# Kernel optimization log

Measured on AMD Instinct MI355X. Metric: run time of the kernel, lower is better.

The kernel has to match this reference:

```python
import jax, jax.numpy as jnp
import numpy as np

A = 14      # num abnormalities (hardcoded 14 W_Q Linears)
QD = 64     # query_dim
H = 12      # num_heads
CH = 768    # cls_hidden_dim == H * QD (required by residual add)
B = 4096    # batch


def _layernorm(x, g, b, eps=1e-5):
    m = jnp.mean(x, axis=-1, keepdims=True)
    v = jnp.mean((x - m) ** 2, axis=-1, keepdims=True)
    return (x - m) * jax.lax.rsqrt(v + eps) * g + b


def setup_inputs() -> dict:
    key = jax.random.key(0)
    ks = jax.random.split(key, 9)
    s = 0.02
    return dict(
        classification_queries=jax.random.normal(ks[0], (A, QD), dtype=jnp.float32),
        cls_token=jax.random.normal(ks[1], (B, A, CH), dtype=jnp.float32),
        WQ=jax.random.normal(ks[2], (A, QD, QD), dtype=jnp.float32) * s,  # 14 per-abnormality query projections
        bQ=jnp.zeros((A, QD), dtype=jnp.float32),
        WK=jax.random.normal(ks[3], (H, CH, QD), dtype=jnp.float32) * s,  # per-head K projections
        bK=jnp.zeros((H, QD), dtype=jnp.float32),
        WV=jax.random.normal(ks[4], (H, CH, QD), dtype=jnp.float32) * s,  # per-head V projections
        bV=jnp.zeros((H, QD), dtype=jnp.float32),
        W1=jax.random.normal(ks[5], (H * QD, CH), dtype=jnp.float32) * s,
        b1=jnp.zeros((CH,), dtype=jnp.float32),
        W2=jax.random.normal(ks[6], (CH, CH), dtype=jnp.float32) * s,
        b2=jnp.zeros((CH,), dtype=jnp.float32),
        g1=jnp.ones((CH,), dtype=jnp.float32),
        be1=jnp.zeros((CH,), dtype=jnp.float32),
        g2=jnp.ones((CH,), dtype=jnp.float32),
        be2=jnp.zeros((CH,), dtype=jnp.float32),
    )


def reference(classification_queries, cls_token, WQ, bQ, WK, bK, WV, bV,
              W1, b1, W2, b2, g1, be1, g2, be2):
    dt = cls_token.dtype
    scale = jnp.asarray(float(QD) ** 0.5, dt)
    # Per-abnormality query projection (batched over the 14 Linears): [A, QD]
    Q = jnp.einsum('ad,adq->aq', classification_queries, WQ) + bQ
    # Per-head K/V projections, batched over heads: [B, H, S, QD] with S == A == 14
    K = jnp.einsum('bsc,hcq->bhsq', cls_token, WK) + bK[None, :, None, :]
    V = jnp.einsum('bsc,hcq->bhsq', cls_token, WV) + bV[None, :, None, :]
    # Attention scores: [B, H, A, S]; Q is broadcast across batch (torch expand)
    scores = jnp.einsum('aq,bhsq->bhas', Q, K) / scale
    # NOTE: original applies softmax over dim=1 of [B, A, S] -> the query axis 'a'
    attn = jax.nn.softmax(scores, axis=2)
    # Weighted values, heads concatenated on last dim: [B, A, H*QD]
    out = jnp.einsum('bhas,bhsq->bahq', attn, V).reshape(cls_token.shape[0], A, H * QD)
    x = _layernorm(cls_token + out, g1, be1)
    ff = jnp.maximum(jnp.dot(x, W1) + b1, 0.0) @ W2 + b2
    return _layernorm(x + ff, g2, be2)
```

## Files before the change

### kernel.cpp

```cpp
#include <hip/hip_runtime.h>
#include <stdint.h>

#define B_  4096
#define A_  14
#define QD_ 64
#define H_  12
#define CH_ 768
#define M_  (B_*A_)
#define NS_ (H_*A_)
#define N1_ (CH_+NS_)

typedef float  f32x4  __attribute__((ext_vector_type(4)));
typedef short  bf16x8 __attribute__((ext_vector_type(8)));
typedef short  s16x4  __attribute__((ext_vector_type(4)));
typedef int    i32x4  __attribute__((ext_vector_type(4)));

#define GLOAD_LDS16(gp, lp) \
  __builtin_amdgcn_global_load_lds((const __attribute__((address_space(1))) void*)(gp), \
                                   (__attribute__((address_space(3))) void*)(lp), 16, 0, 0)

__device__ __forceinline__ float b2f(ushort u) {
  union { uint32_t u; float f; } c; c.u = ((uint32_t)u) << 16; return c.f;
}
__device__ __forceinline__ ushort f2b(float f) {
  union { float f; uint32_t u; } c; c.f = f;
  uint32_t u = c.u;
  return (ushort)((u + 0x7FFFu + ((u >> 16) & 1u)) >> 16);
}


__global__ void prep_q(const float* __restrict__ cq, const float* __restrict__ WQ,
                       const float* __restrict__ bQ, float* __restrict__ Qout) {
  for (int i = threadIdx.x; i < A_*QD_; i += 256) {
    int a = i >> 6, q = i & 63;
    float acc = bQ[i];
    for (int d = 0; d < 64; ++d) acc += cq[a*64 + d] * WQ[(a*64 + d)*64 + q];
    Qout[i] = acc;
  }
}

__global__ void prep_wcat(const float* __restrict__ WV, const float* __restrict__ bV,
                          const float* __restrict__ WK, const float* __restrict__ bK,
                          const float* __restrict__ Qb, ushort* __restrict__ Wcat,
                          float* __restrict__ biascat) {
  int n = blockIdx.x, t = threadIdx.x;
  if (n < CH_) {
    int h = n >> 6, q = n & 63;
    for (int c = t; c < CH_; c += 256)
      Wcat[(size_t)n*CH_ + c] = f2b(WV[((size_t)h*CH_ + c)*64 + q]);
    if (t == 0) biascat[n] = bV[n];
  } else if (n < N1_) {
    int j = n - CH_; int h = j / 14, a = j % 14;
    __shared__ float qrow[64];
    if (t < 64) qrow[t] = Qb[a*64 + t];
    __syncthreads();
    for (int c = t; c < CH_; c += 256) {
      const float* wk = WK + ((size_t)h*CH_ + c)*64;
      float acc = 0.f;
      #pragma unroll
      for (int q = 0; q < 64; ++q) acc += qrow[q] * wk[q];
      Wcat[(size_t)n*CH_ + c] = f2b(acc * 0.125f);
    }
    if (t == 0) {
      float acc = 0.f;
      for (int q = 0; q < 64; ++q) acc += qrow[q] * bK[h*64 + q];
      biascat[n] = acc * 0.125f;
    }
  } else {
    for (int c = t; c < CH_; c += 256) Wcat[(size_t)n*CH_ + c] = 0;
    if (t == 0) biascat[n] = 0.f;
  }
}

__global__ void prep_wt(const float* __restrict__ W1, const float* __restrict__ W2,
                        ushort* __restrict__ W1T, ushort* __restrict__ W2T) {
  int i = blockIdx.x;
  int n = (i < CH_) ? i : i - CH_;
  const float* W = (i < CH_) ? W1 : W2;
  ushort* O = (i < CH_) ? W1T : W2T;
  for (int k = threadIdx.x; k < CH_; k += 256)
    O[(size_t)n*CH_ + k] = f2b(W[(size_t)k*CH_ + n]);
}

__global__ void prep_cls(const float* __restrict__ cls, ushort* __restrict__ out) {
  const size_t n4 = (size_t)M_*CH_/4;
  for (size_t i = (size_t)blockIdx.x*256 + threadIdx.x; i < n4; i += (size_t)gridDim.x*256) {
    const float* p = cls + i*4;
    s16x4 o;
    o[0] = (short)f2b(p[0]); o[1] = (short)f2b(p[1]);
    o[2] = (short)f2b(p[2]); o[3] = (short)f2b(p[3]);
    *(s16x4*)(out + i*4) = o;
  }
}

template<int MODE>
__global__ __launch_bounds__(512, 2)
void gemm_k(const ushort* __restrict__ Ap, const ushort* __restrict__ Bp,
            const float* __restrict__ bias,
            ushort* __restrict__ Cb, float* __restrict__ Sout) {
  constexpr int GN  = (MODE == 0) ? 4 : 3;
  constexpr int NWG = 224 * GN;
  const int tid = threadIdx.x;
  const int wave = tid >> 6, lane = tid & 63;
  const int wm = wave >> 2, wn = wave & 3;

  const int bid = blockIdx.x;
  const int tl = (bid & 7) * (NWG >> 3) + (bid >> 3);
  const int m0 = (tl / GN) * 256, n0 = (tl % GN) * 256;

  __shared__ __align__(16) ushort Asm[2][256*64];
  __shared__ __align__(16) ushort Bsm[2][256*64];

  f32x4 acc[8][4] = {};

  const int tq = tid >> 3;
  const int gsc = (tid & 7) ^ (tq & 7);
  const ushort* Ab = Ap + (size_t)(m0 + tq)*CH_ + gsc*8;
  const ushort* Bb = Bp + (size_t)(n0 + tq)*CH_ + gsc*8;

  #define STAGE_TILE(slot, k0) do {                                         \
    _Pragma("unroll")                                                       \
    for (int q = 0; q < 4; ++q) {                                           \
      GLOAD_LDS16(Ab + (size_t)q*64*CH_ + (k0), &Asm[slot][q*4096 + wave*512]); \
      GLOAD_LDS16(Bb + (size_t)q*64*CH_ + (k0), &Bsm[slot][q*4096 + wave*512]); \
    }                                                                       \
  } while (0)

  STAGE_TILE(0, 0);

  for (int kt = 0; kt < 12; ++kt) {
    const int cur = kt & 1;
    if (kt < 11) {
      STAGE_TILE(cur ^ 1, (kt + 1) * 64);
      asm volatile("s_waitcnt vmcnt(8)" ::: "memory");
    } else {
      asm volatile("s_waitcnt vmcnt(0)" ::: "memory");
    }
    __builtin_amdgcn_sched_barrier(0);
    __builtin_amdgcn_s_barrier();
    __builtin_amdgcn_sched_barrier(0);

    const ushort* As = &Asm[cur][0];
    const ushort* Bs = &Bsm[cur][0];
    #pragma unroll
    for (int kk = 0; kk < 2; ++kk) {
      bf16x8 af[8], bfr[4];
      #pragma unroll
      for (int i = 0; i < 8; ++i) {
        int ar = wm*128 + i*16 + (lane & 15);
        int ab = (ar*128 + kk*64 + (lane >> 4)*16) ^ ((ar & 7) << 4);
        af[i] = *(const bf16x8*)((const char*)As + ab);
      }
      #pragma unroll
      for (int j = 0; j < 4; ++j) {
        int br = wn*64 + j*16 + (lane & 15);
        int bb = (br*128 + kk*64 + (lane >> 4)*16) ^ ((br & 7) << 4);
        bfr[j] = *(const bf16x8*)((const char*)Bs + bb);
      }
      __builtin_amdgcn_s_setprio(1);
      #pragma unroll
      for (int i = 0; i < 8; ++i)
        #pragma unroll
        for (int j = 0; j < 4; ++j)
          acc[i][j] = __builtin_amdgcn_mfma_f32_16x16x32_bf16(af[i], bfr[j], acc[i][j], 0, 0, 0);
      __builtin_amdgcn_s_setprio(0);
    }
    __builtin_amdgcn_sched_barrier(0);
    __builtin_amdgcn_s_barrier();
    __builtin_amdgcn_sched_barrier(0);
  }
  #undef STAGE_TILE

  #pragma unroll
  for (int j = 0; j < 4; ++j) {
    const int gc = n0 + wn*64 + j*16 + (lane & 15);
    const float bv = (MODE == 0 && gc >= N1_) ? 0.f : bias[gc];
    #pragma unroll
    for (int i = 0; i < 8; ++i) {
      const int gr0 = m0 + wm*128 + i*16 + ((lane >> 4) << 2);
      #pragma unroll
      for (int r = 0; r < 4; ++r) {
        const float v = acc[i][j][r] + bv;
        const int gr = gr0 + r;
        if (MODE == 0) {
          if (gc < CH_) {
            Cb[(size_t)gr*CH_ + gc] = f2b(v);
          } else if (gc < N1_) {
            const int j2 = gc - CH_;
            const int h = j2 / 14, a = j2 % 14;
            const int b = gr / 14, s = gr % 14;
            Sout[(((size_t)b*H_ + h)*A_ + a)*A_ + s] = v;
          }
        } else if (MODE == 1) {
          Cb[(size_t)gr*CH_ + gc] = f2b(fmaxf(v, 0.f));
        } else {
          Cb[(size_t)gr*CH_ + gc] = f2b(v);
        }
      }
    }
  }
}

__global__ __launch_bounds__(256)
void attn_ln1(const float* __restrict__ Sbuf, const ushort* __restrict__ Vbuf,
              const ushort* __restrict__ clsb, const float* __restrict__ g1,
              const float* __restrict__ be1, ushort* __restrict__ xout) {
  const int b = blockIdx.x, tid = threadIdx.x;
  const int wave = tid >> 6, lane = tid & 63;
  __shared__ __align__(16) float  s_sc[H_*A_*A_];
  __shared__ __align__(16) ushort s_v[A_*CH_];

  for (int i = tid; i < H_*A_*A_; i += 256) s_sc[i] = Sbuf[(size_t)b*H_*A_*A_ + i];
  for (int i = tid; i < A_*CH_/8; i += 256)
    *(i32x4*)((char*)s_v + i*16) = *(const i32x4*)((const char*)(Vbuf + (size_t)b*A_*CH_) + i*16);
  __syncthreads();

  if (tid < H_*A_) {
    int h = tid / 14, s = tid % 14;
    float vals[14], mx = -1e30f;
    #pragma unroll
    for (int a = 0; a < 14; ++a) { float v = s_sc[(h*14 + a)*14 + s]; vals[a] = v; mx = fmaxf(mx, v); }
    float sum = 0.f;
    #pragma unroll
    for (int a = 0; a < 14; ++a) { float e = __expf(vals[a] - mx); vals[a] = e; sum += e; }
    float inv = 1.f / sum;
    #pragma unroll
    for (int a = 0; a < 14; ++a) s_sc[(h*14 + a)*14 + s] = vals[a] * inv;
  }
  __syncthreads();

  for (int a = wave; a < A_; a += 4) {
    f32x4 vr[3]; float sum = 0.f, sq = 0.f;
    #pragma unroll
    for (int j = 0; j < 3; ++j) {
      const int c = (lane + j*64) * 4;
      const int h = c >> 6;
      const float* at = &s_sc[(h*14 + a)*14];
      f32x4 acc = {};
      #pragma unroll
      for (int s = 0; s < 14; ++s) {
        float w = at[s];
        s16x4 vv = *(const s16x4*)(&s_v[s*CH_ + c]);
        acc[0] += w * b2f((ushort)vv[0]); acc[1] += w * b2f((ushort)vv[1]);
        acc[2] += w * b2f((ushort)vv[2]); acc[3] += w * b2f((ushort)vv[3]);
      }
      s16x4 cv = *(const s16x4*)(clsb + ((size_t)b*A_ + a)*CH_ + c);
      f32x4 t;
      t[0] = b2f((ushort)cv[0]) + acc[0]; t[1] = b2f((ushort)cv[1]) + acc[1];
      t[2] = b2f((ushort)cv[2]) + acc[2]; t[3] = b2f((ushort)cv[3]) + acc[3];
      vr[j] = t;
      #pragma unroll
      for (int u = 0; u < 4; ++u) { sum += t[u]; sq += t[u]*t[u]; }
    }
    #pragma unroll
    for (int off = 32; off >= 1; off >>= 1) {
      sum += __shfl_xor(sum, off, 64);
      sq  += __shfl_xor(sq,  off, 64);
    }
    float mean = sum * (1.f/768.f);
    float var  = sq * (1.f/768.f) - mean*mean;
    float rstd = rsqrtf(var + 1e-5f);
    #pragma unroll
    for (int j = 0; j < 3; ++j) {
      int c = (lane + j*64)*4;
      f32x4 gv = *(const f32x4*)(g1 + c);
      f32x4 bv = *(const f32x4*)(be1 + c);
      s16x4 pk;
      #pragma unroll
      for (int u = 0; u < 4; ++u)
        pk[u] = (short)f2b((vr[j][u] - mean)*rstd*gv[u] + bv[u]);
      *(s16x4*)(&xout[((size_t)b*A_ + a)*CH_ + c]) = pk;
    }
  }
}

__global__ __launch_bounds__(256)
void ln2_k(const ushort* __restrict__ xb, const ushort* __restrict__ yb,
           const float* __restrict__ g2, const float* __restrict__ be2,
           float* __restrict__ out) {
  const int row = blockIdx.x*4 + (threadIdx.x >> 6);
  const int lane = threadIdx.x & 63;
  const ushort* xr = xb + (size_t)row*CH_;
  const ushort* yr = yb + (size_t)row*CH_;
  float v[12]; float sum = 0.f, sq = 0.f;
  #pragma unroll
  for (int j = 0; j < 3; ++j) {
    int c = (lane + j*64)*4;
    s16x4 xv = *(const s16x4*)(xr + c);
    s16x4 yv = *(const s16x4*)(yr + c);
    #pragma unroll
    for (int u = 0; u < 4; ++u) {
      float t = b2f((ushort)xv[u]) + b2f((ushort)yv[u]);
      v[j*4 + u] = t; sum += t; sq += t*t;
    }
  }
  #pragma unroll
  for (int off = 32; off >= 1; off >>= 1) {
    sum += __shfl_xor(sum, off, 64);
    sq  += __shfl_xor(sq,  off, 64);
  }
  float mean = sum * (1.f/768.f);
  float var  = sq * (1.f/768.f) - mean*mean;
  float rstd = rsqrtf(var + 1e-5f);
  float* orow = out + (size_t)row*CH_;
  #pragma unroll
  for (int j = 0; j < 3; ++j) {
    int c = (lane + j*64)*4;
    f32x4 gv = *(const f32x4*)(g2 + c);
    f32x4 bv = *(const f32x4*)(be2 + c);
    f32x4 o;
    #pragma unroll
    for (int u = 0; u < 4; ++u) o[u] = (v[j*4+u] - mean)*rstd*gv[u] + bv[u];
    *(f32x4*)(orow + c) = o;
  }
}

extern "C" void kernel_launch(void* const* d_in, const int* in_sizes, int n_in,
                              void* d_out, int out_size, void* d_ws, size_t ws_size,
                              hipStream_t stream) {
  const float* cq  = (const float*)d_in[0];
  const float* cls = (const float*)d_in[1];
  const float* WQ  = (const float*)d_in[2];
  const float* bQ  = (const float*)d_in[3];
  const float* WK  = (const float*)d_in[4];
  const float* bK  = (const float*)d_in[5];
  const float* WV  = (const float*)d_in[6];
  const float* bV  = (const float*)d_in[7];
  const float* W1  = (const float*)d_in[8];
  const float* b1  = (const float*)d_in[9];
  const float* W2  = (const float*)d_in[10];
  const float* b2  = (const float*)d_in[11];
  const float* g1  = (const float*)d_in[12];
  const float* be1 = (const float*)d_in[13];
  const float* g2  = (const float*)d_in[14];
  const float* be2 = (const float*)d_in[15];
  float* out = (float*)d_out;

  char* ws = (char*)d_ws;
  float*  qbuf    = (float*)(ws + 0);
  float*  biascat = (float*)(ws + 4096);
  ushort* wcat    = (ushort*)(ws + 8192);
  ushort* w1t     = (ushort*)(ws + 1581056);
  ushort* w2t     = (ushort*)(ws + 2760704);
  ushort* clsbf   = (ushort*)(ws + 4194304);
  ushort* vbuf    = (ushort*)(ws + 92274688);
  float*  sbuf    = (float*)(ws + 180355072);
  ushort* ybuf    = (ushort*)(ws + 218890240);
  ushort* xbuf  = clsbf;
  ushort* h1buf = vbuf;

  prep_q   <<<1,    256, 0, stream>>>(cq, WQ, bQ, qbuf);
  prep_wcat<<<1024, 256, 0, stream>>>(WV, bV, WK, bK, qbuf, wcat, biascat);
  prep_wt  <<<1536, 256, 0, stream>>>(W1, W2, w1t, w2t);
  prep_cls <<<2048, 256, 0, stream>>>(cls, clsbf);

  gemm_k<0><<<224*4, 512, 0, stream>>>(clsbf, wcat, biascat, vbuf, sbuf);
  attn_ln1 <<<B_, 256, 0, stream>>>(sbuf, vbuf, clsbf, g1, be1, xbuf);
  gemm_k<1><<<224*3, 512, 0, stream>>>(xbuf, w1t, b1, h1buf, nullptr);
  gemm_k<2><<<224*3, 512, 0, stream>>>(h1buf, w2t, b2, ybuf, nullptr);
  ln2_k    <<<M_/4, 256, 0, stream>>>(xbuf, ybuf, g2, be2, out);
}
```

Before: 740.4 us.

## Switch GEMM mainloop to triple-buffered K=32 tiles with interleaved prefetch

```diff
diff --git a/kernel.cpp b/kernel.cpp
--- a/kernel.cpp
+++ b/kernel.cpp
@@ -100,6 +100,7 @@
             ushort* __restrict__ Cb, float* __restrict__ Sout) {
   constexpr int GN  = (MODE == 0) ? 4 : 3;
   constexpr int NWG = 224 * GN;
+  constexpr int KT  = 24;
   const int tid = threadIdx.x;
   const int wave = tid >> 6, lane = tid & 63;
   const int wm = wave >> 2, wn = wave & 3;
@@ -108,68 +109,79 @@
   const int tl = (bid & 7) * (NWG >> 3) + (bid >> 3);
   const int m0 = (tl / GN) * 256, n0 = (tl % GN) * 256;
 
-  __shared__ __align__(16) ushort Asm[2][256*64];
-  __shared__ __align__(16) ushort Bsm[2][256*64];
+  __shared__ __align__(16) ushort Asm[3][256*32];
+  __shared__ __align__(16) ushort Bsm[3][256*32];
 
   f32x4 acc[8][4] = {};
 
-  const int tq = tid >> 3;
-  const int gsc = (tid & 7) ^ (tq & 7);
-  const ushort* Ab = Ap + (size_t)(m0 + tq)*CH_ + gsc*8;
-  const ushort* Bb = Bp + (size_t)(n0 + tq)*CH_ + gsc*8;
-
-  #define STAGE_TILE(slot, k0) do {                                         \
-    _Pragma("unroll")                                                       \
-    for (int q = 0; q < 4; ++q) {                                           \
-      GLOAD_LDS16(Ab + (size_t)q*64*CH_ + (k0), &Asm[slot][q*4096 + wave*512]); \
-      GLOAD_LDS16(Bb + (size_t)q*64*CH_ + (k0), &Bsm[slot][q*4096 + wave*512]); \
-    }                                                                       \
+  const int line0 = (wave*2 + 0)*8 + (lane >> 3);
+  const int line1 = (wave*2 + 1)*8 + (lane >> 3);
+  const int chS0 = (lane & 7) ^ (line0 & 7);
+  const int chS1 = (lane & 7) ^ (line1 & 7);
+  const int aoff0 = (2*line0 + (chS0 >> 2))*CH_ + (chS0 & 3)*8;
+  const int aoff1 = (2*line1 + (chS1 >> 2))*CH_ + (chS1 & 3)*8;
+  const ushort* Apb = Ap + (size_t)m0*CH_;
+  const ushort* Bpb = Bp + (size_t)n0*CH_;
+
+  #define STAGE_A(slot, k0) do { \
+    GLOAD_LDS16(Apb + aoff0 + (k0), &Asm[slot][(wave*2+0)*512]); \
+    GLOAD_LDS16(Apb + aoff1 + (k0), &Asm[slot][(wave*2+1)*512]); } while (0)
+  #define STAGE_B(slot, k0) do { \
+    GLOAD_LDS16(Bpb + aoff0 + (k0), &Bsm[slot][(wave*2+0)*512]); \
+    GLOAD_LDS16(Bpb + aoff1 + (k0), &Bsm[slot][(wave*2+1)*512]); } while (0)
+
+  const int c0 = lane >> 4;
+  #define FRAG(base, r) (*(const bf16x8*)((const char*)(base) + \
+      ((r) >> 1)*128 + (((((r) & 1) << 2) | c0) ^ (((r) >> 1) & 7))*16))
+
+  STAGE_A(0, 0);  STAGE_B(0, 0);
+  STAGE_A(1, 32); STAGE_B(1, 32);
+
+  const int arow = (lane & 15);
+
+  #define TILE_BODY(T, S) do {                                               \
+    if ((T) == KT-1) { asm volatile("s_waitcnt vmcnt(0)" ::: "memory"); }    \
+    else             { asm volatile("s_waitcnt vmcnt(4)" ::: "memory"); }    \
+    __builtin_amdgcn_sched_barrier(0);                                       \
+    __builtin_amdgcn_s_barrier();                                            \
+    const ushort* As = &Asm[S][0];                                           \
+    const ushort* Bs = &Bsm[S][0];                                           \
+                  \
+    if ((T) < KT-2) STAGE_A(((S)+2)%3, ((T)+2)*32);                          \
+    bf16x8 bfr[4], af[4];                                                    \
+    _Pragma("unroll")                                                        \
+    for (int j = 0; j < 4; ++j) bfr[j] = FRAG(Bs, wn*64 + j*16 + arow);      \
+    _Pragma("unroll")                                                        \
+    for (int i = 0; i < 4; ++i) af[i] = FRAG(As, wm*128 + i*16 + arow);      \
+    __builtin_amdgcn_s_setprio(1);                                           \
+    _Pragma("unroll")                                                        \
+    for (int i = 0; i < 4; ++i)                                              \
+      _Pragma("unroll")                                                      \
+      for (int j = 0; j < 4; ++j)                                            \
+        acc[i][j] = __builtin_amdgcn_mfma_f32_16x16x32_bf16(af[i], bfr[j], acc[i][j], 0, 0, 0); \
+    __builtin_amdgcn_s_setprio(0);                                           \
+                        \
+    if ((T) < KT-2) STAGE_B(((S)+2)%3, ((T)+2)*32);                          \
+    _Pragma("unroll")                                                        \
+    for (int i = 0; i < 4; ++i) af[i] = FRAG(As, wm*128 + 64 + i*16 + arow); \
+    __builtin_amdgcn_s_setprio(1);                                           \
+    _Pragma("unroll")                                                        \
+    for (int i = 0; i < 4; ++i)                                              \
+      _Pragma("unroll")                                                      \
+      for (int j = 0; j < 4; ++j)                                            \
+        acc[4+i][j] = __builtin_amdgcn_mfma_f32_16x16x32_bf16(af[i], bfr[j], acc[4+i][j], 0, 0, 0); \
+    __builtin_amdgcn_s_setprio(0);                                           \
   } while (0)
 
-  STAGE_TILE(0, 0);
-
-  for (int kt = 0; kt < 12; ++kt) {
-    const int cur = kt & 1;
-    if (kt < 11) {
-      STAGE_TILE(cur ^ 1, (kt + 1) * 64);
-      asm volatile("s_waitcnt vmcnt(8)" ::: "memory");
-    } else {
-      asm volatile("s_waitcnt vmcnt(0)" ::: "memory");
-    }
-    __builtin_amdgcn_sched_barrier(0);
-    __builtin_amdgcn_s_barrier();
-    __builtin_amdgcn_sched_barrier(0);
-
-    const ushort* As = &Asm[cur][0];
-    const ushort* Bs = &Bsm[cur][0];
-    #pragma unroll
-    for (int kk = 0; kk < 2; ++kk) {
-      bf16x8 af[8], bfr[4];
-      #pragma unroll
-      for (int i = 0; i < 8; ++i) {
-        int ar = wm*128 + i*16 + (lane & 15);
-        int ab = (ar*128 + kk*64 + (lane >> 4)*16) ^ ((ar & 7) << 4);
-        af[i] = *(const bf16x8*)((const char*)As + ab);
-      }
-      #pragma unroll
-      for (int j = 0; j < 4; ++j) {
-        int br = wn*64 + j*16 + (lane & 15);
-        int bb = (br*128 + kk*64 + (lane >> 4)*16) ^ ((br & 7) << 4);
-        bfr[j] = *(const bf16x8*)((const char*)Bs + bb);
-      }
-      __builtin_amdgcn_s_setprio(1);
-      #pragma unroll
-      for (int i = 0; i < 8; ++i)
-        #pragma unroll
-        for (int j = 0; j < 4; ++j)
-          acc[i][j] = __builtin_amdgcn_mfma_f32_16x16x32_bf16(af[i], bfr[j], acc[i][j], 0, 0, 0);
-      __builtin_amdgcn_s_setprio(0);
-    }
-    __builtin_amdgcn_sched_barrier(0);
-    __builtin_amdgcn_s_barrier();
-    __builtin_amdgcn_sched_barrier(0);
-  }
-  #undef STAGE_TILE
+  for (int tb = 0; tb < KT; tb += 3) {
+    TILE_BODY(tb + 0, 0);
+    TILE_BODY(tb + 1, 1);
+    TILE_BODY(tb + 2, 2);
+  }
+  #undef TILE_BODY
+  #undef STAGE_A
+  #undef STAGE_B
+  #undef FRAG
 
   #pragma unroll
   for (int j = 0; j < 4; ++j) {
```

Measured after the change: 721.4 us. 2.6% less time.
